# Optimization experiments

Hardware: AMD Instinct MI355X
Metric: run time of the kernel (lower is better)

## Reference

```python
import jax, jax.numpy as jnp
import numpy as np

B, L = 2, 1024
DIM = 512
N_LAYERS = 2
D_STATE = 16
D_CONV = 4
D_INNER = 2 * DIM          # expand_factor=2
DT_RANK = (DIM + 15) // 16  # ceil(d_model/16) = 32
VOCAB = 32000


def _rmsnorm(x, w, eps=1e-5):
    return x * jax.lax.rsqrt(jnp.mean(x * x, axis=-1, keepdims=True) + eps) * w


def _causal_conv(x, w, b):
    # x: (B,L,D_INNER); depthwise causal conv along L, kernel D_CONV
    xt = jnp.transpose(x, (0, 2, 1))  # (B,C,L)
    y = jax.lax.conv_general_dilated(
        xt, w, window_strides=(1,), padding=[(D_CONV - 1, 0)],
        dimension_numbers=('NCH', 'OIH', 'NCH'), feature_group_count=D_INNER)
    return jnp.transpose(y, (0, 2, 1)) + b


def _ssm(x, xproj_w, dt_w, dt_b, A_log, Dp):
    # x: (B,L,D_INNER)
    A = -jnp.exp(A_log)  # (D_INNER, D_STATE)
    dbc = jnp.einsum('bld,rd->blr', x, xproj_w)  # (B,L,DT_RANK+2*D_STATE)
    delta = jax.nn.softplus(jnp.einsum('blr,dr->bld', dbc[..., :DT_RANK], dt_w) + dt_b)
    Bm = dbc[..., DT_RANK:DT_RANK + D_STATE]   # (B,L,D_STATE)
    Cm = dbc[..., DT_RANK + D_STATE:]          # (B,L,D_STATE)
    dA = jnp.exp(delta[..., None] * A)                       # (B,L,D_INNER,D_STATE)
    dBx = (delta * x)[..., None] * Bm[:, :, None, :]         # (B,L,D_INNER,D_STATE)

    def step(h, inp):
        a, b = inp
        h = a * h + b
        return h, h

    h0 = jnp.zeros((x.shape[0], D_INNER, D_STATE), x.dtype)
    _, hs = jax.lax.scan(step, h0, (jnp.swapaxes(dA, 0, 1), jnp.swapaxes(dBx, 0, 1)))
    y = jnp.einsum('lbds,bls->bld', hs, Cm) + Dp * x
    return y


def _block(h, rw, iw, cw, cb, xw, dw, db, Al, Dp, ow):
    r = _rmsnorm(h, rw)
    xz = jnp.einsum('bld,ed->ble', r, iw)  # (B,L,2*D_INNER)
    xin, z = jnp.split(xz, 2, axis=-1)
    xin = jax.nn.silu(_causal_conv(xin, cw, cb))
    y = _ssm(xin, xw, dw, db, Al, Dp) * jax.nn.silu(z)
    return h + jnp.einsum('ble,de->bld', y, ow)


def _forward(x, embed, rms_w, in_w, conv_w, conv_b, xproj_w, dt_w, dt_b, A_log, Dp, out_w, ln_g, ln_b, head_w, head_b):
    h = embed[x]  # (B,L,DIM)
    for l in range(N_LAYERS):
        h = _block(h, rms_w[l], in_w[l], conv_w[l], conv_b[l], xproj_w[l],
                   dt_w[l], dt_b[l], A_log[l], Dp[l], out_w[l])
    mu = jnp.mean(h, axis=-1, keepdims=True)
    var = jnp.mean((h - mu) ** 2, axis=-1, keepdims=True)
    hn = (h - mu) * jax.lax.rsqrt(var + 1e-5) * ln_g + ln_b
    return jnp.einsum('bld,vd->blv', hn, head_w) + head_b


def setup_inputs() -> dict:
    key = jax.random.key(0)
    ks = jax.random.split(key, 10)
    s = 0.02
    x = jax.random.randint(ks[0], (B, L), 0, VOCAB)
    embed = jax.random.normal(ks[1], (VOCAB, DIM), jnp.float32) * s
    rms_w = jnp.ones((N_LAYERS, DIM), jnp.float32)
    in_w = jax.random.normal(ks[2], (N_LAYERS, 2 * D_INNER, DIM), jnp.float32) * s
    conv_w = jax.random.normal(ks[3], (N_LAYERS, D_INNER, 1, D_CONV), jnp.float32) * s
    conv_b = jnp.zeros((N_LAYERS, D_INNER), jnp.float32)
    xproj_w = jax.random.normal(ks[4], (N_LAYERS, DT_RANK + 2 * D_STATE, D_INNER), jnp.float32) * s
    dt_w = jax.random.normal(ks[5], (N_LAYERS, D_INNER, DT_RANK), jnp.float32) * s
    dt_b = jax.random.normal(ks[6], (N_LAYERS, D_INNER), jnp.float32) * s
    A_log = jnp.log(jnp.broadcast_to(jnp.arange(1, D_STATE + 1, dtype=jnp.float32), (N_LAYERS, D_INNER, D_STATE)))
    Dp = jnp.ones((N_LAYERS, D_INNER), jnp.float32)
    out_w = jax.random.normal(ks[7], (N_LAYERS, DIM, D_INNER), jnp.float32) * s
    ln_g = jnp.ones((DIM,), jnp.float32)
    ln_b = jnp.zeros((DIM,), jnp.float32)
    head_w = jax.random.normal(ks[8], (VOCAB, DIM), jnp.float32) * s
    head_b = jnp.zeros((VOCAB,), jnp.float32)
    return dict(x=x, embed=embed, rms_w=rms_w, in_w=in_w, conv_w=conv_w, conv_b=conv_b,
                xproj_w=xproj_w, dt_w=dt_w, dt_b=dt_b, A_log=A_log, Dp=Dp, out_w=out_w,
                ln_g=ln_g, ln_b=ln_b, head_w=head_w, head_b=head_b)


def reference(x, embed, rms_w, in_w, conv_w, conv_b, xproj_w, dt_w, dt_b, A_log, Dp, out_w, ln_g, ln_b, head_w, head_b):
    return _forward(x, embed, rms_w, in_w, conv_w, conv_b, xproj_w, dt_w, dt_b,
                    A_log, Dp, out_w, ln_g, ln_b, head_w, head_b)
```

## Files before the change

### kernel.cpp

```cpp
#include <hip/hip_runtime.h>

typedef unsigned short u16;
typedef __attribute__((ext_vector_type(8))) __bf16 bf16x8;
typedef __attribute__((ext_vector_type(4))) float f32x4;

#define B_ 2
#define L_ 1024
#define DIM_ 512
#define DINNER_ 1024
#define DSTATE_ 16
#define DTRANK_ 32
#define VOCAB_ 32000
#define NCHUNK 64
#define CLEN 16

__device__ __forceinline__ u16 f2bf(float f) {
    union { float f; unsigned u; } x; x.f = f;
    unsigned r = x.u + 0x7FFFu + ((x.u >> 16) & 1u);
    return (u16)(r >> 16);
}

__global__ __launch_bounds__(256) void prep(const float* __restrict__ in_w,
                                            const float* __restrict__ out_w,
                                            const float* __restrict__ head_w,
                                            const float* __restrict__ dt_w,
                                            const int* __restrict__ x,
                                            const float* __restrict__ embed,
                                            const float* __restrict__ rw,
                                            u16* __restrict__ win,
                                            u16* __restrict__ wout,
                                            u16* __restrict__ whd,
                                            float* __restrict__ dtwT,
                                            float* __restrict__ h,
                                            u16* __restrict__ rbf) {
    int bk = blockIdx.x;
    int t = threadIdx.x;
    if (bk < 19072) {
        const int n1 = 524288;
        const int n2 = n1 + 262144;
        int i = bk * 256 + t;
        const float4* s; ushort4* d; int j;
        if (i < n1)      { s = (const float4*)in_w;   d = (ushort4*)win;  j = i; }
        else if (i < n2) { s = (const float4*)out_w;  d = (ushort4*)wout; j = i - n1; }
        else             { s = (const float4*)head_w; d = (ushort4*)whd;  j = i - n2; }
        float4 v = s[j];
        ushort4 o; o.x = f2bf(v.x); o.y = f2bf(v.y); o.z = f2bf(v.z); o.w = f2bf(v.w);
        d[j] = o;
    } else if (bk < 19328) {
        int bb = bk - 19072;
        int l = bb >> 7;
        int e = (bb & 127) * 256 + t;
        int r = e >> 10, d = e & 1023;
        dtwT[(size_t)l * 32768 + r * 1024 + d] = dt_w[(size_t)l * 32768 + d * 32 + r];
    } else {
        int wave = t >> 6, lane = t & 63;
        int row = (bk - 19328) * 4 + wave;
        int tok = x[row];
        const float4* s = (const float4*)(embed + (size_t)tok * DIM_);
        float4 v0 = s[lane], v1 = s[lane + 64];
        float4* hd = (float4*)(h + (size_t)row * DIM_);
        hd[lane] = v0;
        hd[lane + 64] = v1;
        float ss = v0.x*v0.x + v0.y*v0.y + v0.z*v0.z + v0.w*v0.w
                 + v1.x*v1.x + v1.y*v1.y + v1.z*v1.z + v1.w*v1.w;
        for (int m = 1; m < 64; m <<= 1) ss += __shfl_xor(ss, m);
        float rms = rsqrtf(ss * (1.0f / DIM_) + 1e-5f);
        const float4* w4 = (const float4*)rw;
        float4 w0 = w4[lane], w1 = w4[lane + 64];
        u16* o = rbf + (size_t)row * DIM_;
        ushort4 a, b;
        a.x = f2bf(v0.x * rms * w0.x); a.y = f2bf(v0.y * rms * w0.y);
        a.z = f2bf(v0.z * rms * w0.z); a.w = f2bf(v0.w * rms * w0.w);
        b.x = f2bf(v1.x * rms * w1.x); b.y = f2bf(v1.y * rms * w1.y);
        b.z = f2bf(v1.z * rms * w1.z); b.w = f2bf(v1.w * rms * w1.w);
        *(ushort4*)(o + lane * 4) = a;
        *(ushort4*)(o + 256 + lane * 4) = b;
    }
}

__global__ __launch_bounds__(256) void rmsnorm_bf16(const float* __restrict__ h,
                                                    const float* __restrict__ w,
                                                    u16* __restrict__ out) {
    int wave = threadIdx.x >> 6, lane = threadIdx.x & 63;
    int row = blockIdx.x * 4 + wave;
    const float4* r4 = (const float4*)(h + (size_t)row * DIM_);
    float4 v0 = r4[lane], v1 = r4[lane + 64];
    float ss = v0.x*v0.x + v0.y*v0.y + v0.z*v0.z + v0.w*v0.w
             + v1.x*v1.x + v1.y*v1.y + v1.z*v1.z + v1.w*v1.w;
    for (int m = 1; m < 64; m <<= 1) ss += __shfl_xor(ss, m);
    float rms = rsqrtf(ss * (1.0f / DIM_) + 1e-5f);
    const float4* w4 = (const float4*)w;
    float4 w0 = w4[lane], w1 = w4[lane + 64];
    u16* o = out + (size_t)row * DIM_;
    ushort4 a, b;
    a.x = f2bf(v0.x * rms * w0.x); a.y = f2bf(v0.y * rms * w0.y);
    a.z = f2bf(v0.z * rms * w0.z); a.w = f2bf(v0.w * rms * w0.w);
    b.x = f2bf(v1.x * rms * w1.x); b.y = f2bf(v1.y * rms * w1.y);
    b.z = f2bf(v1.z * rms * w1.z); b.w = f2bf(v1.w * rms * w1.w);
    *(ushort4*)(o + lane * 4) = a;
    *(ushort4*)(o + 256 + lane * 4) = b;
}

__global__ __launch_bounds__(256) void layernorm_bf16(const float* __restrict__ h,
                                                      const float* __restrict__ g,
                                                      const float* __restrict__ bta,
                                                      u16* __restrict__ out) {
    int wave = threadIdx.x >> 6, lane = threadIdx.x & 63;
    int row = blockIdx.x * 4 + wave;
    const float4* r4 = (const float4*)(h + (size_t)row * DIM_);
    float4 v0 = r4[lane], v1 = r4[lane + 64];
    float s = v0.x + v0.y + v0.z + v0.w + v1.x + v1.y + v1.z + v1.w;
    float ss = v0.x*v0.x + v0.y*v0.y + v0.z*v0.z + v0.w*v0.w
             + v1.x*v1.x + v1.y*v1.y + v1.z*v1.z + v1.w*v1.w;
    for (int m = 1; m < 64; m <<= 1) { s += __shfl_xor(s, m); ss += __shfl_xor(ss, m); }
    float mu = s * (1.0f / DIM_);
    float var = ss * (1.0f / DIM_) - mu * mu;
    float rs = rsqrtf(var + 1e-5f);
    const float4* g4 = (const float4*)g;
    const float4* b4 = (const float4*)bta;
    float4 g0 = g4[lane], g1 = g4[lane + 64];
    float4 b0 = b4[lane], b1 = b4[lane + 64];
    u16* o = out + (size_t)row * DIM_;
    ushort4 a, b;
    a.x = f2bf((v0.x - mu) * rs * g0.x + b0.x); a.y = f2bf((v0.y - mu) * rs * g0.y + b0.y);
    a.z = f2bf((v0.z - mu) * rs * g0.z + b0.z); a.w = f2bf((v0.w - mu) * rs * g0.w + b0.w);
    b.x = f2bf((v1.x - mu) * rs * g1.x + b1.x); b.y = f2bf((v1.y - mu) * rs * g1.y + b1.y);
    b.z = f2bf((v1.z - mu) * rs * g1.z + b1.z); b.w = f2bf((v1.w - mu) * rs * g1.w + b1.w);
    *(ushort4*)(o + lane * 4) = a;
    *(ushort4*)(o + 256 + lane * 4) = b;
}

template <int MODE>
__global__ __launch_bounds__(256) void gemm_bt(const u16* __restrict__ A,
                                               const u16* __restrict__ B,
                                               float* __restrict__ C,
                                               const float* __restrict__ bias,
                                               int M, int N, int K,
                                               int nbx, int swzq) {
    __shared__ u16 As[2][128 * 64];
    __shared__ u16 Bs[2][128 * 64];
    const int tid = threadIdx.x;
    const int wave = tid >> 6;
    const int lane = tid & 63;
    int lin = blockIdx.x;
    if (swzq) lin = (lin & 7) * swzq + (lin >> 3);
    const int m0 = (lin % nbx) * 128;
    const int n0 = (lin / nbx) * 128;
    const int wr = wave >> 1, wc = wave & 1;
    f32x4 acc[4][4] = {};

    const int crow = lane >> 3;
    const int scol = ((lane & 7) ^ crow) * 8;

    auto stage = [&](int buf, int k0) {
        #pragma unroll
        for (int i = 0; i < 8; ++i) {
            int c = wave * 8 + i;
            const u16* src;
            u16* dst;
            if (c < 16) {
                int row = c * 8 + crow;
                src = A + (size_t)(m0 + row) * K + k0 + scol;
                dst = &As[buf][c * 512];
            } else {
                int cc = c - 16;
                int row = cc * 8 + crow;
                src = B + (size_t)(n0 + row) * K + k0 + scol;
                dst = &Bs[buf][cc * 512];
            }
            __builtin_amdgcn_global_load_lds((const __attribute__((address_space(1))) void*)src,
                                             (__attribute__((address_space(3))) void*)dst,
                                             16, 0, 0);
        }
    };

    const int nt = K / 64;
    stage(0, 0);
    __syncthreads();
    int cur = 0;
    const int fr = lane & 15;
    const int q = lane >> 4;
    for (int t = 0; t < nt; ++t) {
        if (t + 1 < nt) stage(cur ^ 1, (t + 1) * 64);
        bf16x8 a[2][4], b[2][4];
        #pragma unroll
        for (int ki = 0; ki < 2; ++ki) {
            #pragma unroll
            for (int mi = 0; mi < 4; ++mi) {
                int row = wr * 64 + mi * 16 + fr;
                a[ki][mi] = *(const bf16x8*)(&As[cur][row * 64 + ((((ki << 2) + q) ^ (fr & 7)) * 8)]);
            }
            #pragma unroll
            for (int ni = 0; ni < 4; ++ni) {
                int row = wc * 64 + ni * 16 + fr;
                b[ki][ni] = *(const bf16x8*)(&Bs[cur][row * 64 + ((((ki << 2) + q) ^ (fr & 7)) * 8)]);
            }
        }
        #pragma unroll
        for (int ki = 0; ki < 2; ++ki)
            #pragma unroll
            for (int mi = 0; mi < 4; ++mi)
                #pragma unroll
                for (int ni = 0; ni < 4; ++ni)
                    acc[mi][ni] = __builtin_amdgcn_mfma_f32_16x16x32_bf16(a[ki][mi], b[ki][ni], acc[mi][ni], 0, 0, 0);
        __syncthreads();
        cur ^= 1;
    }

    const int cl = lane & 15;
    const int rq = (lane >> 4) * 4;
    #pragma unroll
    for (int mi = 0; mi < 4; ++mi) {
        #pragma unroll
        for (int ni = 0; ni < 4; ++ni) {
            int col = n0 + wc * 64 + ni * 16 + cl;
            #pragma unroll
            for (int rr = 0; rr < 4; ++rr) {
                int row = m0 + wr * 64 + mi * 16 + rq + rr;
                size_t idx = (size_t)row * N + col;
                float v = acc[mi][ni][rr];
                if (MODE == 2)      C[idx] = v + bias[col];
                else                C[idx] = v;
            }
        }
    }
}

template <int MODE>
__global__ __launch_bounds__(256) void gemm64(const u16* __restrict__ A,
                                              const u16* __restrict__ B,
                                              float* __restrict__ C,
                                              int M, int N, int K,
                                              int nbx, int swzq) {
    __shared__ u16 As[2][64 * 64];
    __shared__ u16 Bs[2][64 * 64];
    const int tid = threadIdx.x;
    const int wave = tid >> 6;
    const int lane = tid & 63;
    int lin = blockIdx.x;
    if (swzq) lin = (lin & 7) * swzq + (lin >> 3);
    const int m0 = (lin % nbx) * 64;
    const int n0 = (lin / nbx) * 64;
    const int wr = wave >> 1, wc = wave & 1;
    f32x4 acc[2][2] = {};

    const int crow = lane >> 3;
    const int scol = ((lane & 7) ^ crow) * 8;

    auto stage = [&](int buf, int k0) {
        #pragma unroll
        for (int i = 0; i < 4; ++i) {
            int c = wave * 4 + i;
            const u16* src;
            u16* dst;
            if (c < 8) {
                int row = c * 8 + crow;
                src = A + (size_t)(m0 + row) * K + k0 + scol;
                dst = &As[buf][c * 512];
            } else {
                int cc = c - 8;
                int row = cc * 8 + crow;
                src = B + (size_t)(n0 + row) * K + k0 + scol;
                dst = &Bs[buf][cc * 512];
            }
            __builtin_amdgcn_global_load_lds((const __attribute__((address_space(1))) void*)src,
                                             (__attribute__((address_space(3))) void*)dst,
                                             16, 0, 0);
        }
    };

    const int nt = K / 64;
    stage(0, 0);
    __syncthreads();
    int cur = 0;
    const int fr = lane & 15;
    const int q = lane >> 4;
    for (int t = 0; t < nt; ++t) {
        if (t + 1 < nt) stage(cur ^ 1, (t + 1) * 64);
        bf16x8 a[2][2], b[2][2];
        #pragma unroll
        for (int ki = 0; ki < 2; ++ki) {
            #pragma unroll
            for (int mi = 0; mi < 2; ++mi) {
                int row = wr * 32 + mi * 16 + fr;
                a[ki][mi] = *(const bf16x8*)(&As[cur][row * 64 + ((((ki << 2) + q) ^ (fr & 7)) * 8)]);
            }
            #pragma unroll
            for (int ni = 0; ni < 2; ++ni) {
                int row = wc * 32 + ni * 16 + fr;
                b[ki][ni] = *(const bf16x8*)(&Bs[cur][row * 64 + ((((ki << 2) + q) ^ (fr & 7)) * 8)]);
            }
        }
        #pragma unroll
        for (int ki = 0; ki < 2; ++ki)
            #pragma unroll
            for (int mi = 0; mi < 2; ++mi)
                #pragma unroll
                for (int ni = 0; ni < 2; ++ni)
                    acc[mi][ni] = __builtin_amdgcn_mfma_f32_16x16x32_bf16(a[ki][mi], b[ki][ni], acc[mi][ni], 0, 0, 0);
        __syncthreads();
        cur ^= 1;
    }

    const int cl = lane & 15;
    const int rq = (lane >> 4) * 4;
    #pragma unroll
    for (int mi = 0; mi < 2; ++mi) {
        #pragma unroll
        for (int ni = 0; ni < 2; ++ni) {
            int col = n0 + wc * 32 + ni * 16 + cl;
            #pragma unroll
            for (int rr = 0; rr < 4; ++rr) {
                int row = m0 + wr * 32 + mi * 16 + rq + rr;
                size_t idx = (size_t)row * N + col;
                float v = acc[mi][ni][rr];
                if (MODE == 1)      C[idx] += v;
                else                C[idx] = v;
            }
        }
    }
}

__global__ __launch_bounds__(256) void conv_xproj_dt(const float* __restrict__ xz,
                                                     const float* __restrict__ cw,
                                                     const float* __restrict__ cb,
                                                     const float* __restrict__ xw,
                                                     const float* __restrict__ dtwT,
                                                     const float* __restrict__ dtb,
                                                     float* __restrict__ xc,
                                                     float* __restrict__ dbc,
                                                     float* __restrict__ delta) {
    __shared__ float sxc[8 * 1024];
    __shared__ float sxw[64 * 132];
    __shared__ float sred[4][8][68];
    __shared__ float sdbc[8][64];
    int t = threadIdx.x;
    int m0 = blockIdx.x * 8;
    #pragma unroll
    for (int i = 0; i < 32; ++i) {
        int idx = t + i * 256;
        int mi = idx >> 10, d = idx & 1023;
        int m = m0 + mi;
        int l = m & (L_ - 1);
        float acc = cb[d];
        #pragma unroll
        for (int j = 0; j < 4; ++j) {
            int ll = l - 3 + j;
            if (ll >= 0) acc = fmaf(cw[d * 4 + j], xz[(size_t)(m - 3 + j) * (2 * DINNER_) + d], acc);
        }
        float sv = acc / (1.0f + __expf(-acc));
        sxc[mi * 1024 + d] = sv;
        xc[(size_t)m * DINNER_ + d] = sv;
    }
    const int n = t & 63, kg = t >> 6;
    float acc8[8] = {};
    for (int kc = 0; kc < 8; ++kc) {
        __syncthreads();
        #pragma unroll
        for (int i = 0; i < 8; ++i) {
            int f = t + i * 256;
            int row = f >> 5, col4 = f & 31;
            *(float4*)(&sxw[row * 132 + col4 * 4]) =
                *(const float4*)(xw + (size_t)row * DINNER_ + kc * 128 + col4 * 4);
        }
        __syncthreads();
        #pragma unroll
        for (int k4i = 0; k4i < 8; ++k4i) {
            int k4 = kg * 8 + k4i;
            float4 wv = *(const float4*)(&sxw[n * 132 + k4 * 4]);
            #pragma unroll
            for (int mi = 0; mi < 8; ++mi) {
                float4 xv = *(const float4*)(&sxc[mi * 1024 + kc * 128 + k4 * 4]);
                acc8[mi] += wv.x * xv.x + wv.y * xv.y + wv.z * xv.z + wv.w * xv.w;
            }
        }
    }
    #pragma unroll
    for (int mi = 0; mi < 8; ++mi) sred[kg][mi][n] = acc8[mi];
    __syncthreads();
    #pragma unroll
    for (int rep = 0; rep < 2; ++rep) {
        int o = t + rep * 256;
        int mi = o >> 6, n2 = o & 63;
        float v = sred[0][mi][n2] + sred[1][mi][n2] + sred[2][mi][n2] + sred[3][mi][n2];
        sdbc[mi][n2] = v;
        dbc[(size_t)(m0 + mi) * 64 + n2] = v;
    }
    __syncthreads();
    {
        int d0 = t * 4;
        float4 bias = *(const float4*)(dtb + d0);
        float4 am[8];
        #pragma unroll
        for (int mi = 0; mi < 8; ++mi) am[mi] = bias;
        const float4* wT = (const float4*)dtwT;
        #pragma unroll
        for (int r = 0; r < 32; ++r) {
            float4 wv = wT[r * 256 + t];
            #pragma unroll
            for (int mi = 0; mi < 8; ++mi) {
                float s = sdbc[mi][r];
                am[mi].x = fmaf(s, wv.x, am[mi].x);
                am[mi].y = fmaf(s, wv.y, am[mi].y);
                am[mi].z = fmaf(s, wv.z, am[mi].z);
                am[mi].w = fmaf(s, wv.w, am[mi].w);
            }
        }
        #pragma unroll
        for (int mi = 0; mi < 8; ++mi) {
            float4 o;
            o.x = (am[mi].x > 20.f) ? am[mi].x : log1pf(__expf(am[mi].x));
            o.y = (am[mi].y > 20.f) ? am[mi].y : log1pf(__expf(am[mi].y));
            o.z = (am[mi].z > 20.f) ? am[mi].z : log1pf(__expf(am[mi].z));
            o.w = (am[mi].w > 20.f) ? am[mi].w : log1pf(__expf(am[mi].w));
            *(float4*)(delta + (size_t)(m0 + mi) * DINNER_ + d0) = o;
        }
    }
}

__global__ __launch_bounds__(256) void ssm_part1(const float* __restrict__ delta,
                                                 const float* __restrict__ xc,
                                                 const float* __restrict__ dbc,
                                                 const float* __restrict__ A_log,
                                                 float* __restrict__ hfin,
                                                 float* __restrict__ sumd) {
    int tid = threadIdx.x;
    int d = blockIdx.x * 256 + tid;
    int c = blockIdx.y;
    int b = blockIdx.z;
    __shared__ float sB[CLEN][DSTATE_];
    {
        int l = tid >> 4, s = tid & 15;
        sB[l][s] = dbc[((size_t)(b * L_ + c * CLEN + l)) * 64 + DTRANK_ + s];
    }
    float A[16], h[16];
    {
        const float4* Ar = (const float4*)(A_log + (size_t)d * DSTATE_);
        #pragma unroll
        for (int i = 0; i < 4; ++i) {
            float4 al = Ar[i];
            A[i * 4 + 0] = -__expf(al.x); A[i * 4 + 1] = -__expf(al.y);
            A[i * 4 + 2] = -__expf(al.z); A[i * 4 + 3] = -__expf(al.w);
        }
    }
    #pragma unroll
    for (int s = 0; s < 16; ++s) h[s] = 0.f;
    __syncthreads();
    float sd = 0.f;
    size_t base = ((size_t)b * L_ + c * CLEN) * DINNER_ + d;
    #pragma unroll
    for (int l = 0; l < CLEN; ++l) {
        float dv = delta[base + (size_t)l * DINNER_];
        float xv = xc[base + (size_t)l * DINNER_];
        sd += dv;
        float dx = dv * xv;
        #pragma unroll
        for (int s = 0; s < 16; ++s) {
            float e = __expf(dv * A[s]);
            h[s] = fmaf(e, h[s], dx * sB[l][s]);
        }
    }
    float* hf = hfin + (((size_t)b * NCHUNK + c) * DINNER_ + d) * 16;
    #pragma unroll
    for (int i = 0; i < 4; ++i) {
        float4 v; v.x = h[i*4]; v.y = h[i*4+1]; v.z = h[i*4+2]; v.w = h[i*4+3];
        *(float4*)(hf + i * 4) = v;
    }
    sumd[((size_t)b * NCHUNK + c) * DINNER_ + d] = sd;
}

__global__ __launch_bounds__(256) void ssm_carry(const float* __restrict__ hfin,
                                                 const float* __restrict__ sumd,
                                                 const float* __restrict__ A_log,
                                                 float* __restrict__ h0buf) {
    int t = blockIdx.x * 256 + threadIdx.x;
    int s = t & 15;
    int dg = t >> 4;
    int d = dg & (DINNER_ - 1);
    int b = dg >> 10;
    float As = -__expf(A_log[(size_t)d * DSTATE_ + s]);
    float hc = 0.f;
    #pragma unroll 4
    for (int c = 0; c < NCHUNK; ++c) {
        size_t k = (((size_t)b * NCHUNK + c) * DINNER_ + d) * 16 + s;
        h0buf[k] = hc;
        float sdv = sumd[((size_t)b * NCHUNK + c) * DINNER_ + d];
        float hf = hfin[k];
        hc = fmaf(__expf(As * sdv), hc, hf);
    }
}

__global__ __launch_bounds__(256) void ssm_part2(const float* __restrict__ delta,
                                                 const float* __restrict__ xc,
                                                 const float* __restrict__ dbc,
                                                 const float* __restrict__ xz,
                                                 const float* __restrict__ A_log,
                                                 const float* __restrict__ Dp,
                                                 const float* __restrict__ h0buf,
                                                 u16* __restrict__ ys) {
    int tid = threadIdx.x;
    int d = blockIdx.x * 256 + tid;
    int c = blockIdx.y;
    int b = blockIdx.z;
    __shared__ float sBC[CLEN][32];
    {
        int l = tid >> 5, j = tid & 31;
        sBC[l][j] = dbc[((size_t)(b * L_ + c * CLEN + l)) * 64 + DTRANK_ + j];
        int e1 = tid + 256;
        l = e1 >> 5; j = e1 & 31;
        sBC[l][j] = dbc[((size_t)(b * L_ + c * CLEN + l)) * 64 + DTRANK_ + j];
    }
    float A[16], h[16];
    {
        const float4* Ar = (const float4*)(A_log + (size_t)d * DSTATE_);
        #pragma unroll
        for (int i = 0; i < 4; ++i) {
            float4 al = Ar[i];
            A[i * 4 + 0] = -__expf(al.x); A[i * 4 + 1] = -__expf(al.y);
            A[i * 4 + 2] = -__expf(al.z); A[i * 4 + 3] = -__expf(al.w);
        }
        const float4* h0 = (const float4*)(h0buf + (((size_t)b * NCHUNK + c) * DINNER_ + d) * 16);
        #pragma unroll
        for (int i = 0; i < 4; ++i) {
            float4 v = h0[i];
            h[i * 4 + 0] = v.x; h[i * 4 + 1] = v.y; h[i * 4 + 2] = v.z; h[i * 4 + 3] = v.w;
        }
    }
    float Dval = Dp[d];
    __syncthreads();
    size_t base = ((size_t)b * L_ + c * CLEN) * DINNER_ + d;
    size_t zbase = ((size_t)b * L_ + c * CLEN) * (2 * DINNER_) + DINNER_ + d;
    #pragma unroll
    for (int l = 0; l < CLEN; ++l) {
        float dv = delta[base + (size_t)l * DINNER_];
        float xv = xc[base + (size_t)l * DINNER_];
        float zv = xz[zbase + (size_t)l * (2 * DINNER_)];
        float dx = dv * xv;
        float y = 0.f;
        #pragma unroll
        for (int s = 0; s < 16; ++s) {
            float e = __expf(dv * A[s]);
            h[s] = fmaf(e, h[s], dx * sBC[l][s]);
            y = fmaf(h[s], sBC[l][16 + s], y);
        }
        y = fmaf(Dval, xv, y);
        float sg = zv / (1.0f + __expf(-zv));
        ys[base + (size_t)l * DINNER_] = f2bf(y * sg);
    }
}

extern "C" void kernel_launch(void* const* d_in, const int* in_sizes, int n_in,
                              void* d_out, int out_size, void* d_ws, size_t ws_size,
                              hipStream_t stream) {
    const int*   x       = (const int*)d_in[0];
    const float* embed   = (const float*)d_in[1];
    const float* rms_w   = (const float*)d_in[2];
    const float* in_w    = (const float*)d_in[3];
    const float* conv_w  = (const float*)d_in[4];
    const float* conv_b  = (const float*)d_in[5];
    const float* xproj_w = (const float*)d_in[6];
    const float* dt_w    = (const float*)d_in[7];
    const float* dt_b    = (const float*)d_in[8];
    const float* A_log   = (const float*)d_in[9];
    const float* Dp      = (const float*)d_in[10];
    const float* out_w   = (const float*)d_in[11];
    const float* ln_g    = (const float*)d_in[12];
    const float* ln_b    = (const float*)d_in[13];
    const float* head_w  = (const float*)d_in[14];
    const float* head_b  = (const float*)d_in[15];
    float* out = (float*)d_out;

    char* p = (char*)d_ws;
    auto take = [&](size_t n) { char* q = p; p += (n + 255) & ~(size_t)255; return q; };
    float* h    = (float*)take(2048ull * 512 * 4);
    u16*   r_bf = (u16*)  take(2048ull * 512 * 2);
    float* xz   = (float*)take(2048ull * 2048 * 4);
    float* xc   = (float*)take(2048ull * 1024 * 4);
    float* dbc  = (float*)take(2048ull * 64 * 4);
    float* dlt  = (float*)take(2048ull * 1024 * 4);
    u16*   ys   = (u16*)  take(2048ull * 1024 * 2);
    u16*   hn   = (u16*)  take(2048ull * 512 * 2);
    u16*   win  = (u16*)  take(2ull * 2048 * 512 * 2);
    u16*   wout = (u16*)  take(2ull * 512 * 1024 * 2);
    u16*   whd  = (u16*)  take(32000ull * 512 * 2);
    float* dtwT = (float*)take(2ull * 32 * 1024 * 4);
    float* hfin = (float*)take((size_t)B_ * NCHUNK * DINNER_ * 16 * 4);
    float* h0b  = (float*)take((size_t)B_ * NCHUNK * DINNER_ * 16 * 4);
    float* sumd = (float*)take((size_t)B_ * NCHUNK * DINNER_ * 4);

    prep<<<19840, 256, 0, stream>>>(in_w, out_w, head_w, dt_w, x, embed, rms_w,
                                    win, wout, whd, dtwT, h, r_bf);

    for (int l = 0; l < 2; ++l) {
        if (l > 0) rmsnorm_bf16<<<512, 256, 0, stream>>>(h, rms_w + l * DIM_, r_bf);
        gemm_bt<0><<<256, 256, 0, stream>>>(r_bf, win + (size_t)l * 2048 * 512, xz, nullptr, 2048, 2048, 512, 16, 32);
        conv_xproj_dt<<<256, 256, 0, stream>>>(xz, conv_w + l * DINNER_ * 4, conv_b + l * DINNER_,
                                               xproj_w + (size_t)l * 64 * 1024,
                                               dtwT + (size_t)l * 32 * 1024, dt_b + l * DINNER_,
                                               xc, dbc, dlt);
        ssm_part1<<<dim3(4, NCHUNK, B_), 256, 0, stream>>>(dlt, xc, dbc, A_log + (size_t)l * DINNER_ * DSTATE_, hfin, sumd);
        ssm_carry<<<128, 256, 0, stream>>>(hfin, sumd, A_log + (size_t)l * DINNER_ * DSTATE_, h0b);
        ssm_part2<<<dim3(4, NCHUNK, B_), 256, 0, stream>>>(dlt, xc, dbc, xz, A_log + (size_t)l * DINNER_ * DSTATE_,
                                                           Dp + l * DINNER_, h0b, ys);
        gemm64<1><<<256, 256, 0, stream>>>(ys, wout + (size_t)l * 512 * 1024, h, 2048, 512, 1024, 32, 32);
    }

    layernorm_bf16<<<512, 256, 0, stream>>>(h, ln_g, ln_b, hn);
    gemm_bt<2><<<4000, 256, 0, stream>>>(hn, whd, out, head_b, 2048, VOCAB_, 512, 16, 500);
}
```

Before: 378.3 us.

## Deepen GEMM LDS pipeline to four stages with vmcnt-based waits

```diff
diff --git a/kernel.cpp b/kernel.cpp
--- a/kernel.cpp
+++ b/kernel.cpp
@@ -137,8 +137,8 @@
                                                const float* __restrict__ bias,
                                                int M, int N, int K,
                                                int nbx, int swzq) {
-    __shared__ u16 As[2][128 * 64];
-    __shared__ u16 Bs[2][128 * 64];
+    __shared__ u16 As[4][128 * 32];
+    __shared__ u16 Bs[4][128 * 32];
     const int tid = threadIdx.x;
     const int wave = tid >> 6;
     const int lane = tid & 63;
@@ -149,22 +149,25 @@
     const int wr = wave >> 1, wc = wave & 1;
     f32x4 acc[4][4] = {};
 
-    const int crow = lane >> 3;
-    const int scol = ((lane & 7) ^ crow) * 8;
-
-    auto stage = [&](int buf, int k0) {
-        #pragma unroll
-        for (int i = 0; i < 8; ++i) {
-            int c = wave * 8 + i;
+    const int sub = lane >> 2;
+    const int slotL = lane & 3;
+    const int fsub = (sub & 3) ^ ((sub >> 2) & 3);
+    const int scol = (slotL ^ fsub) * 8;
+
+    auto stage = [&](int buf, int kt) {
+        int k0 = kt * 32;
+        #pragma unroll
+        for (int i = 0; i < 4; ++i) {
+            int c = wave * 4 + i;
             const u16* src;
             u16* dst;
-            if (c < 16) {
-                int row = c * 8 + crow;
+            if (c < 8) {
+                int row = c * 16 + sub;
                 src = A + (size_t)(m0 + row) * K + k0 + scol;
                 dst = &As[buf][c * 512];
             } else {
-                int cc = c - 16;
-                int row = cc * 8 + crow;
+                int cc = c - 8;
+                int row = cc * 16 + sub;
                 src = B + (size_t)(n0 + row) * K + k0 + scol;
                 dst = &Bs[buf][cc * 512];
             }
@@ -174,37 +177,39 @@
         }
     };
 
-    const int nt = K / 64;
-    stage(0, 0);
-    __syncthreads();
-    int cur = 0;
+    const int nt = K / 32;
+    stage(0, 0); stage(1, 1); stage(2, 2);
+
     const int fr = lane & 15;
     const int q = lane >> 4;
+    const int fswz = (fr & 3) ^ ((fr >> 2) & 3);
+    const int rdoff = ((q ^ fswz) * 8);
+
     for (int t = 0; t < nt; ++t) {
-        if (t + 1 < nt) stage(cur ^ 1, (t + 1) * 64);
-        bf16x8 a[2][4], b[2][4];
-        #pragma unroll
-        for (int ki = 0; ki < 2; ++ki) {
-            #pragma unroll
-            for (int mi = 0; mi < 4; ++mi) {
-                int row = wr * 64 + mi * 16 + fr;
-                a[ki][mi] = *(const bf16x8*)(&As[cur][row * 64 + ((((ki << 2) + q) ^ (fr & 7)) * 8)]);
-            }
-            #pragma unroll
-            for (int ni = 0; ni < 4; ++ni) {
-                int row = wc * 64 + ni * 16 + fr;
-                b[ki][ni] = *(const bf16x8*)(&Bs[cur][row * 64 + ((((ki << 2) + q) ^ (fr & 7)) * 8)]);
-            }
-        }
-        #pragma unroll
-        for (int ki = 0; ki < 2; ++ki)
-            #pragma unroll
-            for (int mi = 0; mi < 4; ++mi)
-                #pragma unroll
-                for (int ni = 0; ni < 4; ++ni)
-                    acc[mi][ni] = __builtin_amdgcn_mfma_f32_16x16x32_bf16(a[ki][mi], b[ki][ni], acc[mi][ni], 0, 0, 0);
-        __syncthreads();
-        cur ^= 1;
+        if (t + 2 < nt)      asm volatile("s_waitcnt vmcnt(8)" ::: "memory");
+        else if (t + 1 < nt) asm volatile("s_waitcnt vmcnt(4)" ::: "memory");
+        else                 asm volatile("s_waitcnt vmcnt(0)" ::: "memory");
+        __builtin_amdgcn_sched_barrier(0);
+        __builtin_amdgcn_s_barrier();
+        asm volatile("" ::: "memory");
+        __builtin_amdgcn_sched_barrier(0);
+        if (t + 3 < nt) stage((t + 3) & 3, t + 3);
+        const u16* Ab = &As[t & 3][0];
+        const u16* Bb = &Bs[t & 3][0];
+        bf16x8 a[4], b[4];
+        #pragma unroll
+        for (int mi = 0; mi < 4; ++mi)
+            a[mi] = *(const bf16x8*)(Ab + (wr * 64 + mi * 16 + fr) * 32 + rdoff);
+        #pragma unroll
+        for (int ni = 0; ni < 4; ++ni)
+            b[ni] = *(const bf16x8*)(Bb + (wc * 64 + ni * 16 + fr) * 32 + rdoff);
+        __builtin_amdgcn_s_setprio(1);
+        #pragma unroll
+        for (int mi = 0; mi < 4; ++mi)
+            #pragma unroll
+            for (int ni = 0; ni < 4; ++ni)
+                acc[mi][ni] = __builtin_amdgcn_mfma_f32_16x16x32_bf16(a[mi], b[ni], acc[mi][ni], 0, 0, 0);
+        __builtin_amdgcn_s_setprio(0);
     }
 
     const int cl = lane & 15;
@@ -232,8 +237,8 @@
                                               float* __restrict__ C,
                                               int M, int N, int K,
                                               int nbx, int swzq) {
-    __shared__ u16 As[2][64 * 64];
-    __shared__ u16 Bs[2][64 * 64];
+    __shared__ u16 As[4][64 * 64];
+    __shared__ u16 Bs[4][64 * 64];
     const int tid = threadIdx.x;
     const int wave = tid >> 6;
     const int lane = tid & 63;
@@ -247,7 +252,8 @@
     const int crow = lane >> 3;
     const int scol = ((lane & 7) ^ crow) * 8;
 
-    auto stage = [&](int buf, int k0) {
+    auto stage = [&](int buf, int kt) {
+        int k0 = kt * 64;
         #pragma unroll
         for (int i = 0; i < 4; ++i) {
             int c = wave * 4 + i;
@@ -270,27 +276,37 @@
     };
 
     const int nt = K / 64;
-    stage(0, 0);
-    __syncthreads();
-    int cur = 0;
+    stage(0, 0); stage(1, 1); stage(2, 2);
+
     const int fr = lane & 15;
     const int q = lane >> 4;
+
     for (int t = 0; t < nt; ++t) {
-        if (t + 1 < nt) stage(cur ^ 1, (t + 1) * 64);
+        if (t + 2 < nt)      asm volatile("s_waitcnt vmcnt(8)" ::: "memory");
+        else if (t + 1 < nt) asm volatile("s_waitcnt vmcnt(4)" ::: "memory");
+        else                 asm volatile("s_waitcnt vmcnt(0)" ::: "memory");
+        __builtin_amdgcn_sched_barrier(0);
+        __builtin_amdgcn_s_barrier();
+        asm volatile("" ::: "memory");
+        __builtin_amdgcn_sched_barrier(0);
+        if (t + 3 < nt) stage((t + 3) & 3, t + 3);
+        const u16* Ab = &As[t & 3][0];
+        const u16* Bb = &Bs[t & 3][0];
         bf16x8 a[2][2], b[2][2];
         #pragma unroll
         for (int ki = 0; ki < 2; ++ki) {
             #pragma unroll
             for (int mi = 0; mi < 2; ++mi) {
                 int row = wr * 32 + mi * 16 + fr;
-                a[ki][mi] = *(const bf16x8*)(&As[cur][row * 64 + ((((ki << 2) + q) ^ (fr & 7)) * 8)]);
+                a[ki][mi] = *(const bf16x8*)(Ab + row * 64 + ((((ki << 2) + q) ^ (fr & 7)) * 8));
             }
             #pragma unroll
             for (int ni = 0; ni < 2; ++ni) {
                 int row = wc * 32 + ni * 16 + fr;
-                b[ki][ni] = *(const bf16x8*)(&Bs[cur][row * 64 + ((((ki << 2) + q) ^ (fr & 7)) * 8)]);
-            }
-        }
+                b[ki][ni] = *(const bf16x8*)(Bb + row * 64 + ((((ki << 2) + q) ^ (fr & 7)) * 8));
+            }
+        }
+        __builtin_amdgcn_s_setprio(1);
         #pragma unroll
         for (int ki = 0; ki < 2; ++ki)
             #pragma unroll
@@ -298,8 +314,7 @@
                 #pragma unroll
                 for (int ni = 0; ni < 2; ++ni)
                     acc[mi][ni] = __builtin_amdgcn_mfma_f32_16x16x32_bf16(a[ki][mi], b[ki][ni], acc[mi][ni], 0, 0, 0);
-        __syncthreads();
-        cur ^= 1;
+        __builtin_amdgcn_s_setprio(0);
     }
 
     const int cl = lane & 15;
```

After: 373.9 us. About the same (-1.2%).
